# Kernel optimization log

Hardware: AMD Instinct MI355X
Metric: run time of the kernel (lower is better)

The kernel has to match this reference:

```python
import jax, jax.numpy as jnp
import numpy as np

BSZ, L, H, P = 4, 4096, 1024, 512
DT_MIN, DT_MAX = 1e-3, 1e-1


def setup_inputs() -> dict:
    key = jax.random.key(0)
    ks = jax.random.split(key, 6)
    input_sequence = jax.random.normal(ks[0], (BSZ, 1, H, 1, L), jnp.float32)
    # hidden_state_method='zero': hiddens arg only has to carry the right shape
    hiddens = jnp.zeros((BSZ, 1, P), jnp.float32)
    # stable (left-half-plane) diagonal state matrix, like HiPPO-LegS eigenvalues
    Lambda_re = -0.5 * jax.random.uniform(ks[1], (P,), jnp.float32) - 0.1
    Lambda_im = jnp.pi * jnp.arange(P, dtype=jnp.float32)
    # B stored as (P, H, 2) real/imag pair (lecun-ish scale), C as (H, P, 2)
    B = jax.random.normal(ks[2], (P, H, 2), jnp.float32) / jnp.sqrt(2.0 * H)
    C = jax.random.normal(ks[3], (H, P, 2), jnp.float32) / jnp.sqrt(2.0 * P)
    D = jax.random.normal(ks[4], (H,), jnp.float32)
    log_step = jax.random.uniform(ks[5], (P, 1), jnp.float32,
                                  minval=float(np.log(DT_MIN)),
                                  maxval=float(np.log(DT_MAX)))
    return dict(input_sequence=input_sequence, hiddens=hiddens,
                Lambda_re=Lambda_re, Lambda_im=Lambda_im,
                B=B, C=C, D=D, log_step=log_step)


def _binop(qi, qj):
    # diagonal linear recurrence combine: x_j = A_j * x_i + b_j
    Ai, bi = qi
    Aj, bj = qj
    return (Aj * Ai, Aj * bi + bj)


def _s5_forward(input_sequence, Lambda_re, Lambda_im, B, C, D, log_step):
    Lam = jax.lax.complex(Lambda_re, Lambda_im)              # (P,)
    step = jnp.exp(log_step[:, 0])                           # (P,)
    # zero-order-hold discretization
    Lambda_bar = jnp.exp(Lam * step)                         # (P,) complex
    B_scale = (Lambda_bar - 1.0) / Lam                       # (P,) complex
    B_bar_re = B_scale.real[:, None] * B[..., 0] - B_scale.imag[:, None] * B[..., 1]
    B_bar_im = B_scale.real[:, None] * B[..., 1] + B_scale.imag[:, None] * B[..., 0]

    u = input_sequence[:, 0, :, 0].transpose(0, 2, 1)        # (BSZ, L, H) float32

    # Bu_t = B_bar @ u_t, done on real/imag parts to keep u real in the GEMM
    Bu = jax.lax.complex(jnp.einsum('blh,ph->blp', u, B_bar_re),
                         jnp.einsum('blh,ph->blp', u, B_bar_im))  # (BSZ,L,P)
    # prepend zero hidden state (hidden_state_method='zero')
    zeros0 = jnp.zeros((Bu.shape[0], 1, Bu.shape[2]), Bu.dtype)
    Bu_elems = jnp.concatenate([zeros0, Bu], axis=1)          # (BSZ,L+1,P)
    Lam_elems = jnp.broadcast_to(Lambda_bar, Bu_elems.shape)  # (BSZ,L+1,P)

    _, xs = jax.lax.associative_scan(_binop, (Lam_elems, Bu_elems), axis=1)
    xs = xs[:, 1:]                                            # (BSZ,L,P) complex states

    # conj_sym=True: y_t = 2 * Re(C_tilde @ x_t)
    Cr, Ci = C[..., 0], C[..., 1]                             # (H,P) each
    ys = 2.0 * (jnp.einsum('hp,blp->blh', Cr, xs.real)
                - jnp.einsum('hp,blp->blh', Ci, xs.imag))     # (BSZ,L,H)
    ys = ys + D * u                                           # feedthrough
    ys = jax.nn.gelu(ys, approximate=False)                   # activation='gelu'
    return ys.transpose(0, 2, 1)[:, None, :, None, :]         # (BSZ,1,H,1,L)


def reference(input_sequence, hiddens, Lambda_re, Lambda_im, B, C, D, log_step):
    del hiddens  # unused with hidden_state_method='zero'
    return _s5_forward(input_sequence, Lambda_re, Lambda_im, B, C, D, log_step)
```

## Files before the change

kernel.cpp:

```cpp
#include <hip/hip_runtime.h>
#include <math.h>


constexpr int kB = 4, kL = 4096, kH = 1024, kP = 512;
constexpr int kM = 1024, kK = 1024, kN = 4096;

typedef short bf16x8 __attribute__((ext_vector_type(8)));
typedef float f32x4 __attribute__((ext_vector_type(4)));

constexpr size_t A1H_OFF = 0;
constexpr size_t A2H_OFF = A1H_OFF + (size_t)kM * kK * 2;
constexpr size_t LBAR_B  = A2H_OFF + (size_t)kM * kK * 2;
constexpr size_t BU_B    = (LBAR_B + 4096 + 255) & ~(size_t)255;
constexpr size_t TH_B    = BU_B + (size_t)kB * kM * kN * 4;
constexpr size_t MID_BYTES = TH_B + (size_t)kB * kN * kK * 2;

__device__ __forceinline__ unsigned short f2bf(float x) {
  unsigned int u = __float_as_uint(x);
  u += 0x7fffu + ((u >> 16) & 1u);
  return (unsigned short)(u >> 16);
}
__device__ __forceinline__ float bf2f(unsigned short h) {
  return __uint_as_float(((unsigned int)h) << 16);
}

__device__ __forceinline__ void gl2lds16(const void* g, void* l) {
  __builtin_amdgcn_global_load_lds(
      (const __attribute__((address_space(1))) void*)g,
      (__attribute__((address_space(3))) void*)l, 16, 0, 0);
}

template <int N>
__device__ __forceinline__ void wait_vm() {
  __builtin_amdgcn_s_waitcnt((N & 15) | ((N >> 4) << 14) | (15 << 8) | (7 << 4));
}

__global__ __launch_bounds__(256) void k_prep12(
    const float* __restrict__ Lre, const float* __restrict__ Lim,
    const float* __restrict__ B, const float* __restrict__ log_step,
    const float* __restrict__ C, unsigned char* __restrict__ ws) {
  int bid = blockIdx.x;
  if (bid < kP) {
    int p = bid;
    float lr = Lre[p], li = Lim[p];
    float step = expf(log_step[p]);
    float er = expf(lr * step);
    float sb, cb;
    sincosf(li * step, &sb, &cb);
    float lbr = er * cb, lbi = er * sb;
    float nr = lbr - 1.0f, ni = lbi;
    float inv = 1.0f / (lr * lr + li * li);
    float sr = (nr * lr + ni * li) * inv;
    float si = (ni * lr - nr * li) * inv;

    if (threadIdx.x == 0) ((float2*)(ws + LBAR_B))[p] = make_float2(lbr, lbi);

    unsigned short* a1h = (unsigned short*)(ws + A1H_OFF);
    const float* Brow = B + (size_t)p * kH * 2;
    for (int h = threadIdx.x; h < kH; h += 256) {
      float br = Brow[2 * h], bi = Brow[2 * h + 1];
      a1h[(size_t)p * kK + h] = f2bf(sr * br - si * bi);
      a1h[(size_t)(kP + p) * kK + h] = f2bf(sr * bi + si * br);
    }
  } else {
    int h = bid - kP;
    unsigned short* a2h = (unsigned short*)(ws + A2H_OFF);
    for (int k = threadIdx.x; k < kK; k += 256) {
      float v = (k < kP) ? 2.f * C[((size_t)h * kP + k) * 2]
                         : -2.f * C[((size_t)h * kP + (k - kP)) * 2 + 1];
      a2h[(size_t)h * kK + k] = f2bf(v);
    }
  }
}

__global__ __launch_bounds__(256) void k_transpose(
    const float* __restrict__ in, unsigned short* __restrict__ oh) {
  __shared__ float t[64][65];
  int b = blockIdx.z;
  int r0 = blockIdx.y * 64;
  int c0 = blockIdx.x * 64;
  int tid = threadIdx.x;
  const float* src = in + ((size_t)b * 1024 + r0) * 4096 + c0;
  int cc = (tid & 15) * 4, rr = tid >> 4;
#pragma unroll
  for (int i = 0; i < 4; i++) {
    float4 v = *(const float4*)(src + (size_t)(rr + i * 16) * 4096 + cc);
    t[rr + i * 16][cc + 0] = v.x;
    t[rr + i * 16][cc + 1] = v.y;
    t[rr + i * 16][cc + 2] = v.z;
    t[rr + i * 16][cc + 3] = v.w;
  }
  __syncthreads();
  int oc = tid >> 2;
  int og = (tid & 3) * 2;
#pragma unroll
  for (int i = 0; i < 2; i++) {
    int g = og + i;
    unsigned short hv[8];
#pragma unroll
    for (int j = 0; j < 8; j++) hv[j] = f2bf(t[g * 8 + j][oc]);
    size_t ob = ((size_t)b * 4096 + c0 + oc) * 1024 + r0 + g * 8;
    *(uint4*)(oh + ob) = *(uint4*)hv;
  }
}


__device__ __forceinline__ int stage_src_off32(int Dp) {
  int Ds = Dp ^ (((Dp >> 9) & 1) << 5);
  int s = Ds >> 10, d = Ds & 1023;
  int row = (s << 4) + (d >> 6);
  int kk = (d & 63) >> 1;
  return row * kK + kk;
}

#define BAR __builtin_amdgcn_s_barrier()
#define LGKM0                                           \
  do {                                                  \
    asm volatile("s_waitcnt lgkmcnt(0)" ::: "memory");  \
    __builtin_amdgcn_sched_barrier(0);                  \
  } while (0)

template <bool EPI>
__global__ __launch_bounds__(512, 4) void k_gemm2p(
    const unsigned short* __restrict__ Ah, const unsigned short* __restrict__ Bh,
    float* __restrict__ out, const float* __restrict__ u,
    const float* __restrict__ D) {
  __shared__ __align__(16) unsigned char lds[49152];
  constexpr int BUF = 24576;
  constexpr int NKT = kK / 32;

  int b = blockIdx.z;
  int m0 = blockIdx.y * 128, n0 = blockIdx.x * 256;
  int tid = threadIdx.x, w = tid >> 6;
  int q = (tid >> 4) & 3, r = tid & 15;
  int wm = (w >> 2) * 64, wn = (w & 3) * 64;
  int wmrb = (w >> 2) * 4, wnrb = (w & 3) * 4;
  int lane_off = (r * 64 + q * 16) ^ ((r & 8) << 2);

  int d0 = tid << 4;
  int rowk = stage_src_off32(d0);

  const unsigned short* pA = Ah + (size_t)m0 * kK;
  const unsigned short* pB = Bh + (size_t)b * kN * kK + (size_t)n0 * kK;

  f32x4 acc[4][4] = {};

#define STG(KT, LB)                                                       \
  do {                                                                    \
    gl2lds16(pA + (KT) * 32 + rowk, lds + (LB) + d0);                     \
    gl2lds16(pB + (KT) * 32 + rowk, lds + (LB) + 8192 + d0);              \
    gl2lds16(pB + (size_t)128 * kK + (KT) * 32 + rowk,                    \
             lds + (LB) + 16384 + d0);                                    \
  } while (0)

#define COMPUTE(LB)                                                       \
  do {                                                                    \
    bf16x8 a[4], bb[4];                                                   \
    _Pragma("unroll")                                                     \
    for (int mi = 0; mi < 4; mi++)                                        \
      a[mi] = *(const bf16x8*)(lds + (LB) + ((wmrb + mi) << 10) + lane_off); \
    _Pragma("unroll")                                                     \
    for (int nj = 0; nj < 4; nj++)                                        \
      bb[nj] = *(const bf16x8*)(lds + (LB) + 8192 +                       \
                                ((wnrb + nj) << 10) + lane_off);          \
    LGKM0;                                                                \
    __builtin_amdgcn_s_setprio(1);                                        \
    _Pragma("unroll")                                                     \
    for (int mi = 0; mi < 4; mi++)                                        \
      _Pragma("unroll")                                                   \
      for (int nj = 0; nj < 4; nj++)                                      \
        acc[mi][nj] = __builtin_amdgcn_mfma_f32_16x16x32_bf16(            \
            a[mi], bb[nj], acc[mi][nj], 0, 0, 0);                         \
    __builtin_amdgcn_s_setprio(0);                                        \
  } while (0)

  STG(0, 0);
  wait_vm<0>();
  BAR;

  for (int it = 0; it < NKT / 2; ++it) {
    int kt = it * 2;
    if (kt + 1 < NKT) STG(kt + 1, BUF);
    COMPUTE(0);
    wait_vm<0>();
    BAR;
    if (kt + 2 < NKT) STG(kt + 2, 0);
    COMPUTE(BUF);
    wait_vm<0>();
    BAR;
  }
#undef STG
#undef COMPUTE

#pragma unroll
  for (int mi = 0; mi < 4; mi++) {
#pragma unroll
    for (int reg = 0; reg < 4; reg++) {
      int row = m0 + wm + mi * 16 + q * 4 + reg;
      float dv = EPI ? D[row] : 0.f;
#pragma unroll
      for (int ni = 0; ni < 4; ni++) {
        int col = n0 + wn + ni * 16 + r;
        size_t o = ((size_t)b * kM + row) * (size_t)kN + col;
        float v = acc[mi][ni][reg];
        if (EPI) {
          float y = v + dv * u[o];
          v = 0.5f * y * (1.f + erff(y * 0.70710678118654752f));
        }
        out[o] = v;
      }
    }
  }
}

__global__ __launch_bounds__(256) void k_scan(float* __restrict__ bu,
                                              const float2* __restrict__ lbar) {
  int p = blockIdx.x & (kP - 1);
  int b = blockIdx.x >> 9;
  int tid = threadIdx.x, lane = tid & 63, w = tid >> 6;
  float2 lam = lbar[p];
  float* sre = bu + ((size_t)b * kM + p) * (size_t)kN;
  float* sim = sre + (size_t)kP * kN;

  float vr[16], vi[16];
  {
    const float4* pr = (const float4*)(sre + tid * 16);
    const float4* pi = (const float4*)(sim + tid * 16);
#pragma unroll
    for (int i = 0; i < 4; i++) {
      float4 a = pr[i], c = pi[i];
      vr[4 * i] = a.x; vr[4 * i + 1] = a.y; vr[4 * i + 2] = a.z; vr[4 * i + 3] = a.w;
      vi[4 * i] = c.x; vi[4 * i + 1] = c.y; vi[4 * i + 2] = c.z; vi[4 * i + 3] = c.w;
    }
  }

  float xr = 0.f, xi = 0.f;
#pragma unroll
  for (int i = 0; i < 16; i++) {
    float nr2 = fmaf(lam.x, xr, fmaf(-lam.y, xi, vr[i]));
    float ni2 = fmaf(lam.x, xi, fmaf(lam.y, xr, vi[i]));
    xr = nr2; xi = ni2;
  }

  float Ar = lam.x, Ai = lam.y;
#pragma unroll
  for (int s = 0; s < 4; s++) {
    float tr = Ar * Ar - Ai * Ai, ti = 2.f * Ar * Ai;
    Ar = tr; Ai = ti;
  }
  float br = xr, bi = xi;

  for (int off = 1; off < 64; off <<= 1) {
    float pAr = __shfl_up(Ar, off), pAi = __shfl_up(Ai, off);
    float pbr = __shfl_up(br, off), pbi = __shfl_up(bi, off);
    if (lane >= off) {
      float nAr = Ar * pAr - Ai * pAi;
      float nAi = Ar * pAi + Ai * pAr;
      float nbr = Ar * pbr - Ai * pbi + br;
      float nbi = Ar * pbi + Ai * pbr + bi;
      Ar = nAr; Ai = nAi; br = nbr; bi = nbi;
    }
  }

  __shared__ float4 wtot[4];
  if (lane == 63) wtot[w] = make_float4(Ar, Ai, br, bi);
  __syncthreads();

  float eAr = __shfl_up(Ar, 1), eAi = __shfl_up(Ai, 1);
  float ebr = __shfl_up(br, 1), ebi = __shfl_up(bi, 1);
  if (lane == 0) { eAr = 1.f; eAi = 0.f; ebr = 0.f; ebi = 0.f; }

  float pAr = 1.f, pAi = 0.f, pbr = 0.f, pbi = 0.f;
  for (int j = 0; j < w; j++) {
    float4 t = wtot[j];
    float nAr = t.x * pAr - t.y * pAi;
    float nAi = t.x * pAi + t.y * pAr;
    float nbr = t.x * pbr - t.y * pbi + t.z;
    float nbi = t.x * pbi + t.y * pbr + t.w;
    pAr = nAr; pAi = nAi; pbr = nbr; pbi = nbi;
  }

  float initr = eAr * pbr - eAi * pbi + ebr;
  float initi = eAr * pbi + eAi * pbr + ebi;

  xr = initr; xi = initi;
  float4* qr = (float4*)(sre + tid * 16);
  float4* qi = (float4*)(sim + tid * 16);
#pragma unroll
  for (int i = 0; i < 4; i++) {
    float rr[4], ii[4];
#pragma unroll
    for (int j = 0; j < 4; j++) {
      float nr2 = fmaf(lam.x, xr, fmaf(-lam.y, xi, vr[4 * i + j]));
      float ni2 = fmaf(lam.x, xi, fmaf(lam.y, xr, vi[4 * i + j]));
      xr = nr2; xi = ni2; rr[j] = nr2; ii[j] = ni2;
    }
    qr[i] = make_float4(rr[0], rr[1], rr[2], rr[3]);
    qi[i] = make_float4(ii[0], ii[1], ii[2], ii[3]);
  }
}

constexpr size_t OBBAR = 0;
constexpr size_t OLBAR = (size_t)kP * kH;
constexpr size_t OBU = OLBAR + 1024;

__global__ __launch_bounds__(256) void k_precomputeF(
    const float* __restrict__ Lre, const float* __restrict__ Lim,
    const float* __restrict__ B, const float* __restrict__ log_step,
    float2* __restrict__ ws) {
  int p = blockIdx.x;
  float lr = Lre[p], li = Lim[p];
  float step = expf(log_step[p]);
  float er = expf(lr * step);
  float sb, cb;
  sincosf(li * step, &sb, &cb);
  float lbr = er * cb, lbi = er * sb;
  float nr = lbr - 1.0f, ni = lbi;
  float inv = 1.0f / (lr * lr + li * li);
  float sr = (nr * lr + ni * li) * inv;
  float si = (ni * lr - nr * li) * inv;
  if (threadIdx.x == 0) ws[OLBAR + p] = make_float2(lbr, lbi);
  float2* Bbar = ws + OBBAR;
  const float* Brow = B + (size_t)p * kH * 2;
  for (int h = threadIdx.x; h < kH; h += 256) {
    float br = Brow[2 * h], bi = Brow[2 * h + 1];
    Bbar[(size_t)p * kH + h] = make_float2(sr * br - si * bi, sr * bi + si * br);
  }
}

__global__ __launch_bounds__(256) void k_gemm1F(
    const float2* __restrict__ ws_bbar, const float* __restrict__ u,
    float2* __restrict__ Bu) {
  __shared__ float2 As[16][64];
  __shared__ float Bs[16][64];
  int b = blockIdx.z, m0 = blockIdx.y * 64, n0 = blockIdx.x * 64;
  int tid = threadIdx.x, tn = tid & 15, tm = tid >> 4;
  const float* uB = u + (size_t)b * kH * kL;
  float2 acc[4][4];
#pragma unroll
  for (int i = 0; i < 4; i++)
#pragma unroll
    for (int j = 0; j < 4; j++) acc[i][j] = make_float2(0.f, 0.f);
  int ar = tid >> 2, ac = (tid & 3) * 4, bk = tid >> 4, bc = (tid & 15) * 4;
  for (int k0 = 0; k0 < kH; k0 += 16) {
    const float4* src = (const float4*)(ws_bbar + (size_t)(m0 + ar) * kH + k0 + ac);
    float4 v01 = src[0], v23 = src[1];
    As[ac + 0][ar] = make_float2(v01.x, v01.y);
    As[ac + 1][ar] = make_float2(v01.z, v01.w);
    As[ac + 2][ar] = make_float2(v23.x, v23.y);
    As[ac + 3][ar] = make_float2(v23.z, v23.w);
    float4 v = *(const float4*)(uB + (size_t)(k0 + bk) * kL + n0 + bc);
    *(float4*)&Bs[bk][bc] = v;
    __syncthreads();
#pragma unroll
    for (int kk = 0; kk < 16; ++kk) {
      const float4* arow = (const float4*)&As[kk][0];
      float4 a01 = arow[tm * 2 + 0], a23 = arow[tm * 2 + 1];
      float2 a[4] = {make_float2(a01.x, a01.y), make_float2(a01.z, a01.w),
                     make_float2(a23.x, a23.y), make_float2(a23.z, a23.w)};
      float4 bv = ((const float4*)&Bs[kk][0])[tn];
      float bbv[4] = {bv.x, bv.y, bv.z, bv.w};
#pragma unroll
      for (int mi = 0; mi < 4; mi++)
#pragma unroll
        for (int ni = 0; ni < 4; ni++) {
          acc[mi][ni].x = fmaf(a[mi].x, bbv[ni], acc[mi][ni].x);
          acc[mi][ni].y = fmaf(a[mi].y, bbv[ni], acc[mi][ni].y);
        }
    }
    __syncthreads();
  }
  float2* BuB = Bu + (size_t)b * kP * kL;
#pragma unroll
  for (int mi = 0; mi < 4; mi++) {
    int row = m0 + tm * 4 + mi;
    float2* dst = BuB + (size_t)row * kL + n0 + tn * 4;
    ((float4*)dst)[0] = make_float4(acc[mi][0].x, acc[mi][0].y, acc[mi][1].x, acc[mi][1].y);
    ((float4*)dst)[1] = make_float4(acc[mi][2].x, acc[mi][2].y, acc[mi][3].x, acc[mi][3].y);
  }
}

__global__ __launch_bounds__(256) void k_scanF(float2* __restrict__ Bu,
                                               const float2* __restrict__ Lbar) {
  int p = blockIdx.x & (kP - 1);
  int b = blockIdx.x >> 9;
  int tid = threadIdx.x, lane = tid & 63, w = tid >> 6;
  float2 lam = Lbar[p];
  float2* seq = Bu + ((size_t)b * kP + p) * kL;
  float2 v[16];
  const float4* src = (const float4*)(seq + tid * 16);
#pragma unroll
  for (int i = 0; i < 8; i++) {
    float4 t = src[i];
    v[2 * i] = make_float2(t.x, t.y);
    v[2 * i + 1] = make_float2(t.z, t.w);
  }
  float xr = 0.f, xi = 0.f;
#pragma unroll
  for (int i = 0; i < 16; i++) {
    float nr2 = fmaf(lam.x, xr, fmaf(-lam.y, xi, v[i].x));
    float ni2 = fmaf(lam.x, xi, fmaf(lam.y, xr, v[i].y));
    xr = nr2; xi = ni2;
  }
  float Ar = lam.x, Ai = lam.y;
#pragma unroll
  for (int s = 0; s < 4; s++) {
    float tr = Ar * Ar - Ai * Ai, ti = 2.f * Ar * Ai;
    Ar = tr; Ai = ti;
  }
  float br = xr, bi = xi;
  for (int off = 1; off < 64; off <<= 1) {
    float pAr = __shfl_up(Ar, off), pAi = __shfl_up(Ai, off);
    float pbr = __shfl_up(br, off), pbi = __shfl_up(bi, off);
    if (lane >= off) {
      float nAr = Ar * pAr - Ai * pAi, nAi = Ar * pAi + Ai * pAr;
      float nbr = Ar * pbr - Ai * pbi + br, nbi = Ar * pbi + Ai * pbr + bi;
      Ar = nAr; Ai = nAi; br = nbr; bi = nbi;
    }
  }
  __shared__ float4 wtot[4];
  if (lane == 63) wtot[w] = make_float4(Ar, Ai, br, bi);
  __syncthreads();
  float eAr = __shfl_up(Ar, 1), eAi = __shfl_up(Ai, 1);
  float ebr = __shfl_up(br, 1), ebi = __shfl_up(bi, 1);
  if (lane == 0) { eAr = 1.f; eAi = 0.f; ebr = 0.f; ebi = 0.f; }
  float pAr = 1.f, pAi = 0.f, pbr = 0.f, pbi = 0.f;
  for (int j = 0; j < w; j++) {
    float4 t = wtot[j];
    float nAr = t.x * pAr - t.y * pAi, nAi = t.x * pAi + t.y * pAr;
    float nbr = t.x * pbr - t.y * pbi + t.z, nbi = t.x * pbi + t.y * pbr + t.w;
    pAr = nAr; pAi = nAi; pbr = nbr; pbi = nbi;
  }
  float initr = eAr * pbr - eAi * pbi + ebr;
  float initi = eAr * pbi + eAi * pbr + ebi;
  xr = initr; xi = initi;
  float4* dst = (float4*)(seq + tid * 16);
#pragma unroll
  for (int i = 0; i < 8; i++) {
    float nr0 = fmaf(lam.x, xr, fmaf(-lam.y, xi, v[2 * i].x));
    float ni0 = fmaf(lam.x, xi, fmaf(lam.y, xr, v[2 * i].y));
    float nr1 = fmaf(lam.x, nr0, fmaf(-lam.y, ni0, v[2 * i + 1].x));
    float ni1 = fmaf(lam.x, ni0, fmaf(lam.y, nr0, v[2 * i + 1].y));
    dst[i] = make_float4(nr0, ni0, nr1, ni1);
    xr = nr1; xi = ni1;
  }
}

__global__ __launch_bounds__(256) void k_gemm2F(
    const float2* __restrict__ C, const float2* __restrict__ X,
    const float* __restrict__ u, const float* __restrict__ D,
    float* __restrict__ out) {
  __shared__ float2 As[16][64];
  __shared__ float2 Bs[16][64];
  int b = blockIdx.z, m0 = blockIdx.y * 64, n0 = blockIdx.x * 64;
  int tid = threadIdx.x, tn = tid & 15, tm = tid >> 4;
  const float2* Xb = X + (size_t)b * kP * kL;
  float acc[4][4];
#pragma unroll
  for (int i = 0; i < 4; i++)
#pragma unroll
    for (int j = 0; j < 4; j++) acc[i][j] = 0.f;
  int ar = tid >> 2, ac = (tid & 3) * 4, bk = tid >> 4, bc = (tid & 15) * 4;
  for (int k0 = 0; k0 < kP; k0 += 16) {
    const float4* src = (const float4*)(C + (size_t)(m0 + ar) * kP + k0 + ac);
    float4 v01 = src[0], v23 = src[1];
    As[ac + 0][ar] = make_float2(v01.x, v01.y);
    As[ac + 1][ar] = make_float2(v01.z, v01.w);
    As[ac + 2][ar] = make_float2(v23.x, v23.y);
    As[ac + 3][ar] = make_float2(v23.z, v23.w);
    const float4* srcb = (const float4*)(Xb + (size_t)(k0 + bk) * kL + n0 + bc);
    ((float4*)&Bs[bk][bc])[0] = srcb[0];
    ((float4*)&Bs[bk][bc])[1] = srcb[1];
    __syncthreads();
#pragma unroll
    for (int kk = 0; kk < 16; ++kk) {
      const float4* arow = (const float4*)&As[kk][0];
      float4 a01 = arow[tm * 2 + 0], a23 = arow[tm * 2 + 1];
      float2 a[4] = {make_float2(a01.x, a01.y), make_float2(a01.z, a01.w),
                     make_float2(a23.x, a23.y), make_float2(a23.z, a23.w)};
      const float4* brow = (const float4*)&Bs[kk][0];
      float4 b01 = brow[tn * 2 + 0], b23 = brow[tn * 2 + 1];
      float2 bbv[4] = {make_float2(b01.x, b01.y), make_float2(b01.z, b01.w),
                       make_float2(b23.x, b23.y), make_float2(b23.z, b23.w)};
#pragma unroll
      for (int mi = 0; mi < 4; mi++)
#pragma unroll
        for (int ni = 0; ni < 4; ni++) {
          acc[mi][ni] = fmaf(a[mi].x, bbv[ni].x, acc[mi][ni]);
          acc[mi][ni] = fmaf(-a[mi].y, bbv[ni].y, acc[mi][ni]);
        }
    }
    __syncthreads();
  }
#pragma unroll
  for (int mi = 0; mi < 4; mi++) {
    int h = m0 + tm * 4 + mi;
    float d = D[h];
    const float* urow = u + ((size_t)b * kH + h) * kL + n0 + tn * 4;
    float4 uv = *(const float4*)urow;
    float uu[4] = {uv.x, uv.y, uv.z, uv.w};
    float res[4];
#pragma unroll
    for (int ni = 0; ni < 4; ni++) {
      float y = 2.f * acc[mi][ni] + d * uu[ni];
      res[ni] = 0.5f * y * (1.f + erff(y * 0.70710678118654752f));
    }
    float* orow = out + ((size_t)b * kH + h) * kL + n0 + tn * 4;
    *(float4*)orow = make_float4(res[0], res[1], res[2], res[3]);
  }
}

extern "C" void kernel_launch(void* const* d_in, const int* in_sizes, int n_in,
                              void* d_out, int out_size, void* d_ws, size_t ws_size,
                              hipStream_t stream) {
  const float* input_sequence = (const float*)d_in[0];
  const float* Lambda_re = (const float*)d_in[2];
  const float* Lambda_im = (const float*)d_in[3];
  const float* B = (const float*)d_in[4];
  const float* C = (const float*)d_in[5];
  const float* D = (const float*)d_in[6];
  const float* log_step = (const float*)d_in[7];
  float* out = (float*)d_out;

  if (ws_size >= MID_BYTES) {
    unsigned char* ws = (unsigned char*)d_ws;
    unsigned short* a1h = (unsigned short*)(ws + A1H_OFF);
    unsigned short* a2h = (unsigned short*)(ws + A2H_OFF);
    float2* lbar = (float2*)(ws + LBAR_B);
    float* bu = (float*)(ws + BU_B);
    unsigned short* th = (unsigned short*)(ws + TH_B);

    k_prep12<<<dim3(kP + kH), 256, 0, stream>>>(Lambda_re, Lambda_im, B,
                                                log_step, C, ws);

    dim3 tgrid(kL / 64, 1024 / 64, kB);
    dim3 ggrid(kN / 256, kM / 128, kB);

    k_transpose<<<tgrid, 256, 0, stream>>>(input_sequence, th);
    k_gemm2p<false><<<ggrid, 512, 0, stream>>>(a1h, th, bu, nullptr, nullptr);
    k_scan<<<dim3(kB * kP), 256, 0, stream>>>(bu, lbar);
    k_transpose<<<tgrid, 256, 0, stream>>>(bu, th);
    k_gemm2p<true><<<ggrid, 512, 0, stream>>>(a2h, th, out, input_sequence, D);
  } else {
    float2* ws = (float2*)d_ws;
    float2* Bbar = ws + OBBAR;
    float2* Lbar = ws + OLBAR;
    float2* Bu = ws + OBU;
    k_precomputeF<<<dim3(kP), 256, 0, stream>>>(Lambda_re, Lambda_im, B, log_step, ws);
    k_gemm1F<<<dim3(kL / 64, kP / 64, kB), 256, 0, stream>>>(Bbar, input_sequence, Bu);
    k_scanF<<<dim3(kB * kP), 256, 0, stream>>>(Bu, Lbar);
    k_gemm2F<<<dim3(kL / 64, kH / 64, kB), 256, 0, stream>>>(
        (const float2*)C, (const float2*)Bu, input_sequence, D, out);
  }
}
```

Before: 279.1 us.

## Fuse transpose and bf16 conversion into GEMM B-operand staging

Removes the two standalone transpose kernels. The GEMM now reads the fp32 K-major activations directly through registers, converts them to bf16, and writes them into LDS in the swizzled layout. The aim is to cut the extra global write and read of the transposed bf16 copies and two kernel launches. In exchange the main loop gains a register-staged B path, extra VALU conversion work and a single-stage prefetch loop. These may reduce overlap relative to the previous direct-to-LDS loads.

```diff
diff --git a/kernel.cpp b/kernel.cpp
--- a/kernel.cpp
+++ b/kernel.cpp
@@ -19,9 +19,6 @@
   unsigned int u = __float_as_uint(x);
   u += 0x7fffu + ((u >> 16) & 1u);
   return (unsigned short)(u >> 16);
-}
-__device__ __forceinline__ float bf2f(unsigned short h) {
-  return __uint_as_float(((unsigned int)h) << 16);
 }
 
 __device__ __forceinline__ void gl2lds16(const void* g, void* l) {
@@ -73,37 +70,6 @@
   }
 }
 
-__global__ __launch_bounds__(256) void k_transpose(
-    const float* __restrict__ in, unsigned short* __restrict__ oh) {
-  __shared__ float t[64][65];
-  int b = blockIdx.z;
-  int r0 = blockIdx.y * 64;
-  int c0 = blockIdx.x * 64;
-  int tid = threadIdx.x;
-  const float* src = in + ((size_t)b * 1024 + r0) * 4096 + c0;
-  int cc = (tid & 15) * 4, rr = tid >> 4;
-#pragma unroll
-  for (int i = 0; i < 4; i++) {
-    float4 v = *(const float4*)(src + (size_t)(rr + i * 16) * 4096 + cc);
-    t[rr + i * 16][cc + 0] = v.x;
-    t[rr + i * 16][cc + 1] = v.y;
-    t[rr + i * 16][cc + 2] = v.z;
-    t[rr + i * 16][cc + 3] = v.w;
-  }
-  __syncthreads();
-  int oc = tid >> 2;
-  int og = (tid & 3) * 2;
-#pragma unroll
-  for (int i = 0; i < 2; i++) {
-    int g = og + i;
-    unsigned short hv[8];
-#pragma unroll
-    for (int j = 0; j < 8; j++) hv[j] = f2bf(t[g * 8 + j][oc]);
-    size_t ob = ((size_t)b * 4096 + c0 + oc) * 1024 + r0 + g * 8;
-    *(uint4*)(oh + ob) = *(uint4*)hv;
-  }
-}
-
 
 __device__ __forceinline__ int stage_src_off32(int Dp) {
   int Ds = Dp ^ (((Dp >> 9) & 1) << 5);
@@ -113,6 +79,8 @@
   return row * kK + kk;
 }
 
+struct f4x4 { float4 v[4]; };
+
 #define BAR __builtin_amdgcn_s_barrier()
 #define LGKM0                                           \
   do {                                                  \
@@ -121,8 +89,8 @@
   } while (0)
 
 template <bool EPI>
-__global__ __launch_bounds__(512, 4) void k_gemm2p(
-    const unsigned short* __restrict__ Ah, const unsigned short* __restrict__ Bh,
+__global__ __launch_bounds__(512, 4) void k_gemmf(
+    const unsigned short* __restrict__ Ah, const float* __restrict__ S,
     float* __restrict__ out, const float* __restrict__ u,
     const float* __restrict__ D) {
   __shared__ __align__(16) unsigned char lds[49152];
@@ -141,56 +109,86 @@
   int rowk = stage_src_off32(d0);
 
   const unsigned short* pA = Ah + (size_t)m0 * kK;
-  const unsigned short* pB = Bh + (size_t)b * kN * kK + (size_t)n0 * kK;
+  const float* pS = S + (size_t)b * ((size_t)kK * kN) + n0;
+
+  int kg = tid & 7, ng = tid >> 3;
+  int wadr[4];
+#pragma unroll
+  for (int j = 0; j < 4; j++) {
+    int n = ng * 4 + j;
+    int a0 = ((n >> 4) << 10) + (n & 15) * 64 + kg * 8;
+    wadr[j] = a0 ^ ((n & 8) ? 32 : 0);
+  }
+  const float* pSb = pS + (size_t)(kg * 4) * kN + ng * 4;
 
   f32x4 acc[4][4] = {};
 
-#define STG(KT, LB)                                                       \
-  do {                                                                    \
-    gl2lds16(pA + (KT) * 32 + rowk, lds + (LB) + d0);                     \
-    gl2lds16(pB + (KT) * 32 + rowk, lds + (LB) + 8192 + d0);              \
-    gl2lds16(pB + (size_t)128 * kK + (KT) * 32 + rowk,                    \
-             lds + (LB) + 16384 + d0);                                    \
+#define BLOAD(T, KT)                                                    \
+  do {                                                                  \
+    const float* bs_ = pSb + (size_t)(KT) * 32 * kN;                    \
+    _Pragma("unroll")                                                   \
+    for (int i_ = 0; i_ < 4; i_++)                                      \
+      (T).v[i_] = *(const float4*)(bs_ + (size_t)i_ * kN);              \
   } while (0)
 
-#define COMPUTE(LB)                                                       \
-  do {                                                                    \
-    bf16x8 a[4], bb[4];                                                   \
-    _Pragma("unroll")                                                     \
-    for (int mi = 0; mi < 4; mi++)                                        \
-      a[mi] = *(const bf16x8*)(lds + (LB) + ((wmrb + mi) << 10) + lane_off); \
-    _Pragma("unroll")                                                     \
-    for (int nj = 0; nj < 4; nj++)                                        \
-      bb[nj] = *(const bf16x8*)(lds + (LB) + 8192 +                       \
-                                ((wnrb + nj) << 10) + lane_off);          \
-    LGKM0;                                                                \
-    __builtin_amdgcn_s_setprio(1);                                        \
-    _Pragma("unroll")                                                     \
-    for (int mi = 0; mi < 4; mi++)                                        \
-      _Pragma("unroll")                                                   \
-      for (int nj = 0; nj < 4; nj++)                                      \
-        acc[mi][nj] = __builtin_amdgcn_mfma_f32_16x16x32_bf16(            \
-            a[mi], bb[nj], acc[mi][nj], 0, 0, 0);                         \
-    __builtin_amdgcn_s_setprio(0);                                        \
+#define BWRITE(T, LB)                                                   \
+  do {                                                                  \
+    const float* f0_ = (const float*)&(T).v[0];                         \
+    const float* f1_ = (const float*)&(T).v[1];                         \
+    const float* f2_ = (const float*)&(T).v[2];                         \
+    const float* f3_ = (const float*)&(T).v[3];                         \
+    _Pragma("unroll")                                                   \
+    for (int j_ = 0; j_ < 4; j_++) {                                    \
+      unsigned int lo_ = ((unsigned int)f2bf(f1_[j_]) << 16) | f2bf(f0_[j_]); \
+      unsigned int hi_ = ((unsigned int)f2bf(f3_[j_]) << 16) | f2bf(f2_[j_]); \
+      *(uint2*)(lds + (LB) + 8192 + wadr[j_]) = make_uint2(lo_, hi_);   \
+    }                                                                   \
   } while (0)
 
-  STG(0, 0);
-  wait_vm<0>();
+  {
+    f4x4 t;
+    BLOAD(t, 0);
+    gl2lds16(pA + rowk, lds + d0);
+    wait_vm<0>();
+    BWRITE(t, 0);
+    LGKM0;
+  }
   BAR;
 
-  for (int it = 0; it < NKT / 2; ++it) {
-    int kt = it * 2;
-    if (kt + 1 < NKT) STG(kt + 1, BUF);
-    COMPUTE(0);
+  for (int kt = 0; kt < NKT; ++kt) {
+    int cur = (kt & 1) ? BUF : 0;
+    int nxt = cur ^ BUF;
+    bool pf = (kt + 1 < NKT);
+    f4x4 t;
+    if (pf) {
+      BLOAD(t, kt + 1);
+      gl2lds16(pA + (kt + 1) * 32 + rowk, lds + nxt + d0);
+    }
+    bf16x8 a[4], bb[4];
+#pragma unroll
+    for (int mi = 0; mi < 4; mi++)
+      a[mi] = *(const bf16x8*)(lds + cur + ((wmrb + mi) << 10) + lane_off);
+#pragma unroll
+    for (int nj = 0; nj < 4; nj++)
+      bb[nj] = *(const bf16x8*)(lds + cur + 8192 + ((wnrb + nj) << 10) + lane_off);
+    LGKM0;
+    __builtin_amdgcn_s_setprio(1);
+#pragma unroll
+    for (int mi = 0; mi < 4; mi++)
+#pragma unroll
+      for (int nj = 0; nj < 4; nj++)
+        acc[mi][nj] = __builtin_amdgcn_mfma_f32_16x16x32_bf16(
+            a[mi], bb[nj], acc[mi][nj], 0, 0, 0);
+    __builtin_amdgcn_s_setprio(0);
     wait_vm<0>();
+    if (pf) {
+      BWRITE(t, nxt);
+      LGKM0;
+    }
     BAR;
-    if (kt + 2 < NKT) STG(kt + 2, 0);
-    COMPUTE(BUF);
-    wait_vm<0>();
-    BAR;
-  }
-#undef STG
-#undef COMPUTE
+  }
+#undef BLOAD
+#undef BWRITE
 
 #pragma unroll
   for (int mi = 0; mi < 4; mi++) {
@@ -528,19 +526,16 @@
     unsigned short* a2h = (unsigned short*)(ws + A2H_OFF);
     float2* lbar = (float2*)(ws + LBAR_B);
     float* bu = (float*)(ws + BU_B);
-    unsigned short* th = (unsigned short*)(ws + TH_B);
 
     k_prep12<<<dim3(kP + kH), 256, 0, stream>>>(Lambda_re, Lambda_im, B,
                                                 log_step, C, ws);
 
-    dim3 tgrid(kL / 64, 1024 / 64, kB);
     dim3 ggrid(kN / 256, kM / 128, kB);
 
-    k_transpose<<<tgrid, 256, 0, stream>>>(input_sequence, th);
-    k_gemm2p<false><<<ggrid, 512, 0, stream>>>(a1h, th, bu, nullptr, nullptr);
+    k_gemmf<false><<<ggrid, 512, 0, stream>>>(a1h, input_sequence, bu,
+                                              nullptr, nullptr);
     k_scan<<<dim3(kB * kP), 256, 0, stream>>>(bu, lbar);
-    k_transpose<<<tgrid, 256, 0, stream>>>(bu, th);
-    k_gemm2p<true><<<ggrid, 512, 0, stream>>>(a2h, th, out, input_sequence, D);
+    k_gemmf<true><<<ggrid, 512, 0, stream>>>(a2h, bu, out, input_sequence, D);
   } else {
     float2* ws = (float2*)d_ws;
     float2* Bbar = ws + OBBAR;
```

Result: slower. 317.5 us (+13.8%).

## Switch GEMM K-loop to triple-buffered LDS pipeline with partial vmcnt waits

Applied to the files above, without the earlier changes.

Replaces the double-buffered K loop in the bf16 MFMA GEMM with a three-stage LDS ring, keeping two tiles of global loads in flight. Each iteration waits only until the oldest stage has landed instead of draining all loads. This is meant to hide global-load latency behind the MFMA work. LDS per block grows from 48 KB to 72 KB, which may lower the number of resident blocks per CU, and an extra barrier is added per iteration. The epilogue ends with a fixed buffer index (BSZ) for the final compute, which depends on NKT matching the ring rotation.

```diff
diff --git a/kernel.cpp b/kernel.cpp
--- a/kernel.cpp
+++ b/kernel.cpp
@@ -19,9 +19,6 @@
   unsigned int u = __float_as_uint(x);
   u += 0x7fffu + ((u >> 16) & 1u);
   return (unsigned short)(u >> 16);
-}
-__device__ __forceinline__ float bf2f(unsigned short h) {
-  return __uint_as_float(((unsigned int)h) << 16);
 }
 
 __device__ __forceinline__ void gl2lds16(const void* g, void* l) {
@@ -121,12 +118,12 @@
   } while (0)
 
 template <bool EPI>
-__global__ __launch_bounds__(512, 4) void k_gemm2p(
+__global__ __launch_bounds__(512, 4) void k_gemm3b(
     const unsigned short* __restrict__ Ah, const unsigned short* __restrict__ Bh,
     float* __restrict__ out, const float* __restrict__ u,
     const float* __restrict__ D) {
-  __shared__ __align__(16) unsigned char lds[49152];
-  constexpr int BUF = 24576;
+  __shared__ __align__(16) unsigned char lds[73728];
+  constexpr int BSZ = 24576;
   constexpr int NKT = kK / 32;
 
   int b = blockIdx.z;
@@ -175,20 +172,27 @@
   } while (0)
 
   STG(0, 0);
+  STG(1, BSZ);
+  wait_vm<3>();
+  BAR;
+
+  int sb = 2 * BSZ;
+  int cb = 0;
+  for (int kt = 0; kt < NKT - 2; ++kt) {
+    STG(kt + 2, sb);
+    wait_vm<6>();
+    BAR;
+    COMPUTE(cb);
+    BAR;
+    sb = (sb == 2 * BSZ) ? 0 : sb + BSZ;
+    cb = (cb == 2 * BSZ) ? 0 : cb + BSZ;
+  }
+  wait_vm<3>();
+  BAR;
+  COMPUTE(cb);
   wait_vm<0>();
   BAR;
-
-  for (int it = 0; it < NKT / 2; ++it) {
-    int kt = it * 2;
-    if (kt + 1 < NKT) STG(kt + 1, BUF);
-    COMPUTE(0);
-    wait_vm<0>();
-    BAR;
-    if (kt + 2 < NKT) STG(kt + 2, 0);
-    COMPUTE(BUF);
-    wait_vm<0>();
-    BAR;
-  }
+  COMPUTE(BSZ);
 #undef STG
 #undef COMPUTE
 
@@ -537,10 +541,10 @@
     dim3 ggrid(kN / 256, kM / 128, kB);
 
     k_transpose<<<tgrid, 256, 0, stream>>>(input_sequence, th);
-    k_gemm2p<false><<<ggrid, 512, 0, stream>>>(a1h, th, bu, nullptr, nullptr);
+    k_gemm3b<false><<<ggrid, 512, 0, stream>>>(a1h, th, bu, nullptr, nullptr);
     k_scan<<<dim3(kB * kP), 256, 0, stream>>>(bu, lbar);
     k_transpose<<<tgrid, 256, 0, stream>>>(bu, th);
-    k_gemm2p<true><<<ggrid, 512, 0, stream>>>(a2h, th, out, input_sequence, D);
+    k_gemm3b<true><<<ggrid, 512, 0, stream>>>(a2h, th, out, input_sequence, D);
   } else {
     float2* ws = (float2*)d_ws;
     float2* Bbar = ws + OBBAR;
```

New measurement: 285.5 us. 1.02x slower.
